# Kernel optimization log

Hardware: AMD Instinct MI355X
Metric: run time of the kernel (lower is better)

The kernel has to match this reference:

```python
import jax, jax.numpy as jnp
import numpy as np

VEC_SIZE = 256
N_VECS = 8
N_CHOICES = 2048
BATCH = 2048
EPS = 1e-6
NAND_BIAS = 3.0


def setup_inputs() -> dict:
    key = jax.random.key(0)
    k1, k2 = jax.random.split(key)
    query = jax.random.normal(k1, (BATCH, N_VECS * VEC_SIZE), dtype=jnp.float32)
    weight = jax.random.normal(k2, (N_CHOICES, VEC_SIZE * N_VECS), dtype=jnp.float32)
    # init code overwrites the randn nand_weight with ones + nand_bias
    nand_weight = jnp.full((N_CHOICES, N_VECS), 1.0 + NAND_BIAS, dtype=jnp.float32)
    return {"query": query, "weight": weight, "nand_weight": nand_weight}


def reference(query, weight, nand_weight):
    # [B, n_vecs, vec_size] and [C, n_vecs, vec_size]
    q = query.reshape(-1, N_VECS, VEC_SIZE)
    w = weight.reshape(-1, N_VECS, VEC_SIZE)
    # torch.cosine_similarity clamps each norm to eps
    qn = q / jnp.maximum(jnp.linalg.norm(q, axis=-1, keepdims=True), EPS)
    wn = w / jnp.maximum(jnp.linalg.norm(w, axis=-1, keepdims=True), EPS)
    # broadcast cosine sim expressed as batched matmul: [B, C, n_vecs]
    cos_sim = jnp.einsum('bnd,cnd->bcn', qn, wn)
    cos_sim = jax.nn.leaky_relu(cos_sim)  # slope 0.01, matches F.leaky_relu default
    nw = jax.nn.sigmoid(nand_weight)[None]  # [1, C, n_vecs]
    interpolated = nw * cos_sim + (1.0 - nw) * (1.0 - cos_sim)
    return jnp.prod(interpolated, axis=2)  # [B, C]
```

## Files before the change

### kernel.cpp

```cpp
#include <hip/hip_runtime.h>
#include <math.h>
#include <stdint.h>

#define BATCH    2048
#define NCHOICES 2048
#define NV       8
#define VS       256
#define KTOT     2048

typedef unsigned short u16;
typedef __attribute__((ext_vector_type(8))) short    bf16x8;
typedef __attribute__((ext_vector_type(8))) u16      u16x8;
typedef __attribute__((ext_vector_type(4))) float    f32x4;

__device__ __forceinline__ u16 f2bf_rne(float x) {
    unsigned u = __float_as_uint(x);
    return (u16)((u + 0x7FFFu + ((u >> 16) & 1u)) >> 16);
}

__global__ __launch_bounds__(256) void prep_convert(
    const float* __restrict__ Q, const float* __restrict__ W,
    const float* __restrict__ NWT,
    u16* __restrict__ Qh, u16* __restrict__ Ql,
    u16* __restrict__ Wh, u16* __restrict__ Wl,
    float* __restrict__ snw)
{
    const int row = blockIdx.x;
    const int t   = threadIdx.x;
    const int n   = t >> 5;
    const int l   = t & 31;

    const float* src; u16 *dh, *dl;
    if (row < BATCH) {
        src = Q + (size_t)row * KTOT;
        dh = Qh + (size_t)row * KTOT; dl = Ql + (size_t)row * KTOT;
    } else {
        src = W + (size_t)(row - BATCH) * KTOT;
        dh = Wh + (size_t)(row - BATCH) * KTOT; dl = Wl + (size_t)(row - BATCH) * KTOT;
    }

    const int idx = n * VS + l * 8;
    float4 x0 = *(const float4*)(src + idx);
    float4 x1 = *(const float4*)(src + idx + 4);
    float xs[8] = {x0.x, x0.y, x0.z, x0.w, x1.x, x1.y, x1.z, x1.w};

    float s = 0.0f;
    #pragma unroll
    for (int j = 0; j < 8; ++j) s = fmaf(xs[j], xs[j], s);
    #pragma unroll
    for (int m = 1; m < 32; m <<= 1) s += __shfl_xor(s, m, 64);
    const float rn = 1.0f / fmaxf(sqrtf(s), 1e-6f);

    u16x8 hv, lv;
    #pragma unroll
    for (int j = 0; j < 8; ++j) {
        float xn = xs[j] * rn;
        u16 h = f2bf_rne(xn);
        float hf = __uint_as_float(((unsigned)h) << 16);
        hv[j] = h;
        lv[j] = f2bf_rne(xn - hf);
    }
    *(u16x8*)(dh + idx) = hv;
    *(u16x8*)(dl + idx) = lv;

    if (row >= BATCH && t < NV) {
        const int c = row - BATCH;
        float x = NWT[(size_t)c * NV + t];
        snw[(size_t)c * NV + t] = 1.0f / (1.0f + expf(-x));
    }
}

__device__ __forceinline__ void gload16(const void* g, void* l) {
    __builtin_amdgcn_global_load_lds(
        (__attribute__((address_space(1))) void*)(uintptr_t)g,
        (__attribute__((address_space(3))) void*)(uint32_t)(uintptr_t)l,
        16, 0, 0);
}

#define RD16(dst, va, OFF) \
    asm volatile("ds_read_b128 %0, %1 offset:" OFF : "=v"(dst) : "v"(va))

__global__ __launch_bounds__(256, 2) void nand_mfma9(
    const u16* __restrict__ Qh, const u16* __restrict__ Ql,
    const u16* __restrict__ Wh, const u16* __restrict__ Wl,
    const float* __restrict__ snw, float* __restrict__ part)
{
    __shared__ __align__(16) u16 L[2][16384];

    const int tid  = threadIdx.x;
    const int lane = tid & 63;
    const int wave = tid >> 6;

    const int f    = blockIdx.x + 16 * blockIdx.y + 256 * blockIdx.z;
    const int virt = (f & 7) * 64 + (f >> 3);
    const int bx   = virt & 15;
    const int by   = (virt >> 4) & 15;
    const int z    = virt >> 8;

    const int wr  = (wave >> 1) * 64;
    const int wc  = (wave & 1) * 64;
    const int bm0 = by * 128;
    const int bn0 = bx * 128;
    const int kb  = z * 1024;

    const int fr = lane & 15;
    const int gi = lane >> 4;

    const int lr = lane >> 2;
    const int sw = 8 * ((lane & 3) ^ ((lane >> 3) & 3));
    const int r0 = wave * 32 + lr;
    const int r1 = r0 + 16;

    const u16* sAh0 = Qh + (size_t)(bm0 + r0) * KTOT + kb + sw;
    const u16* sAh1 = Qh + (size_t)(bm0 + r1) * KTOT + kb + sw;
    const u16* sAl0 = Ql + (size_t)(bm0 + r0) * KTOT + kb + sw;
    const u16* sAl1 = Ql + (size_t)(bm0 + r1) * KTOT + kb + sw;
    const u16* sBh0 = Wh + (size_t)(bn0 + r0) * KTOT + kb + sw;
    const u16* sBh1 = Wh + (size_t)(bn0 + r1) * KTOT + kb + sw;
    const u16* sBl0 = Wl + (size_t)(bn0 + r0) * KTOT + kb + sw;
    const u16* sBl1 = Wl + (size_t)(bn0 + r1) * KTOT + kb + sw;

    #define STAGE(B, T) do { u16* Lb_ = &L[B][0]; const int ko = (T) * 32;   \
        gload16(sAh0 + ko, Lb_ + wave * 1024);                               \
        gload16(sAh1 + ko, Lb_ + wave * 1024 + 512);                         \
        gload16(sAl0 + ko, Lb_ + 4096  + wave * 1024);                       \
        gload16(sAl1 + ko, Lb_ + 4096  + wave * 1024 + 512);                 \
        gload16(sBh0 + ko, Lb_ + 8192  + wave * 1024);                       \
        gload16(sBh1 + ko, Lb_ + 8192  + wave * 1024 + 512);                 \
        gload16(sBl0 + ko, Lb_ + 12288 + wave * 1024);                       \
        gload16(sBl1 + ko, Lb_ + 12288 + wave * 1024 + 512);                 \
    } while (0)

    const uint32_t ldsBase = (uint32_t)(uintptr_t)&L[0][0];
    const uint32_t swz16   = (uint32_t)((gi ^ ((fr >> 1) & 3)) * 16);
    const uint32_t vbaseA  = ldsBase + (uint32_t)((wr + fr) * 64) + swz16;
    const uint32_t vbaseB  = ldsBase + 16384u + (uint32_t)((wc + fr) * 64) + swz16;

    #define MF(AR, BR, M, N) \
        acc[M][N] = __builtin_amdgcn_mfma_f32_16x16x32_bf16(AR[M], BR[N], acc[M][N], 0, 0, 0)
    #define PASS(AR, BR) do {                                                \
        MF(AR, BR, 0, 0); MF(AR, BR, 0, 1); MF(AR, BR, 0, 2); MF(AR, BR, 0, 3); \
        MF(AR, BR, 1, 0); MF(AR, BR, 1, 1); MF(AR, BR, 1, 2); MF(AR, BR, 1, 3); \
        MF(AR, BR, 2, 0); MF(AR, BR, 2, 1); MF(AR, BR, 2, 2); MF(AR, BR, 2, 3); \
        MF(AR, BR, 3, 0); MF(AR, BR, 3, 1); MF(AR, BR, 3, 2); MF(AR, BR, 3, 3); \
    } while (0)

    f32x4 prod[4][4];
    #pragma unroll
    for (int m = 0; m < 4; ++m)
        #pragma unroll
        for (int n = 0; n < 4; ++n) prod[m][n] = (f32x4){1.f, 1.f, 1.f, 1.f};

    STAGE(0, 0);
    asm volatile("s_waitcnt vmcnt(0)");
    __builtin_amdgcn_s_barrier();

    int buf = 0;

    #pragma unroll 1
    for (int cc = 0; cc < 4; ++cc) {
        const int chunk = z * 4 + cc;

        f32x4 acc[4][4];
        #pragma unroll
        for (int m = 0; m < 4; ++m)
            #pragma unroll
            for (int n = 0; n < 4; ++n) acc[m][n] = (f32x4){0.f, 0.f, 0.f, 0.f};

        #pragma unroll 1
        for (int t8 = 0; t8 < 8; ++t8) {
            const int t = cc * 8 + t8;

            if (t + 1 < 32) STAGE(buf ^ 1, t + 1);

            const uint32_t vaA = vbaseA + ((uint32_t)buf << 15);
            const uint32_t vaB = vbaseB + ((uint32_t)buf << 15);

            bf16x8 ah[4], al[4], bh[4], bl[4];
            RD16(ah[0], vaA, "0");     RD16(bh[0], vaB, "0");
            RD16(ah[1], vaA, "1024");  RD16(bh[1], vaB, "1024");
            RD16(ah[2], vaA, "2048");  RD16(bh[2], vaB, "2048");
            RD16(ah[3], vaA, "3072");  RD16(bh[3], vaB, "3072");
            RD16(al[0], vaA, "8192");  RD16(al[1], vaA, "9216");
            RD16(al[2], vaA, "10240"); RD16(al[3], vaA, "11264");
            RD16(bl[0], vaB, "8192");  RD16(bl[1], vaB, "9216");
            RD16(bl[2], vaB, "10240"); RD16(bl[3], vaB, "11264");

            __builtin_amdgcn_s_setprio(1);
            asm volatile("s_waitcnt lgkmcnt(8)");
            __builtin_amdgcn_sched_barrier(0);
            PASS(ah, bh);
            __builtin_amdgcn_sched_barrier(0);
            asm volatile("s_waitcnt lgkmcnt(4)");
            __builtin_amdgcn_sched_barrier(0);
            PASS(al, bh);
            __builtin_amdgcn_sched_barrier(0);
            asm volatile("s_waitcnt lgkmcnt(0)");
            __builtin_amdgcn_sched_barrier(0);
            PASS(ah, bl);
            __builtin_amdgcn_s_setprio(0);

            asm volatile("s_waitcnt vmcnt(0)");
            __builtin_amdgcn_s_barrier();
            buf ^= 1;
        }

        float vv[4], uu[4];
        #pragma unroll
        for (int n = 0; n < 4; ++n) {
            const int col = bn0 + wc + n * 16 + fr;
            float s = snw[(size_t)col * NV + chunk];
            vv[n] = 2.0f * s - 1.0f;
            uu[n] = 1.0f - s;
        }
        #pragma unroll
        for (int m = 0; m < 4; ++m)
            #pragma unroll
            for (int i = 0; i < 4; ++i)
                #pragma unroll
                for (int n = 0; n < 4; ++n) {
                    float cosv = acc[m][n][i];
                    float Lk = fmaxf(cosv, 0.01f * cosv);
                    prod[m][n][i] *= fmaf(Lk, vv[n], uu[n]);
                }
    }

    const int ri = gi * 4;
    float* P = part + (size_t)z * BATCH * NCHOICES;
    #pragma unroll
    for (int m = 0; m < 4; ++m)
        #pragma unroll
        for (int i = 0; i < 4; ++i) {
            const int row = bm0 + wr + m * 16 + ri + i;
            float* pr = P + (size_t)row * NCHOICES + bn0 + wc + fr;
            #pragma unroll
            for (int n = 0; n < 4; ++n) pr[n * 16] = prod[m][n][i];
        }

    #undef STAGE
    #undef MF
    #undef PASS
}

__global__ __launch_bounds__(256) void combine_kernel(
    const float* __restrict__ p, float* __restrict__ out)
{
    const size_t NN = (size_t)BATCH * NCHOICES;
    size_t i = ((size_t)blockIdx.x * 256 + threadIdx.x) * 4;
    float4 a = *(const float4*)(p + i);
    float4 b = *(const float4*)(p + NN + i);
    float4 o;
    o.x = a.x * b.x;
    o.y = a.y * b.y;
    o.z = a.z * b.z;
    o.w = a.w * b.w;
    *(float4*)(out + i) = o;
}

__global__ __launch_bounds__(256) void prep_kernel(
    const float* __restrict__ Q, const float* __restrict__ W,
    const float* __restrict__ NWT,
    float* __restrict__ rq, float* __restrict__ rw, float* __restrict__ snw)
{
    const int row = blockIdx.x;
    const int t   = threadIdx.x;
    const int n   = t >> 5;
    const int l   = t & 31;

    const float* src; float* dst;
    if (row < BATCH) { src = Q + (size_t)row * KTOT; dst = rq + (size_t)row * NV; }
    else { src = W + (size_t)(row - BATCH) * KTOT; dst = rw + (size_t)(row - BATCH) * NV; }

    const float* v = src + n * VS + l * 8;
    float4 a = *(const float4*)(v);
    float4 b = *(const float4*)(v + 4);
    float s = a.x*a.x + a.y*a.y + a.z*a.z + a.w*a.w
            + b.x*b.x + b.y*b.y + b.z*b.z + b.w*b.w;
    #pragma unroll
    for (int m = 1; m < 32; m <<= 1) s += __shfl_xor(s, m, 64);
    if (l == 0) dst[n] = 1.0f / fmaxf(sqrtf(s), 1e-6f);
    if (row >= BATCH && t < NV) {
        const int c = row - BATCH;
        float x = NWT[(size_t)c * NV + t];
        snw[(size_t)c * NV + t] = 1.0f / (1.0f + expf(-x));
    }
}

__global__ __launch_bounds__(256, 2) void nand_gemm(
    const float* __restrict__ Q, const float* __restrict__ W,
    const float* __restrict__ rq, const float* __restrict__ rw,
    const float* __restrict__ snw, float* __restrict__ out)
{
    __shared__ __align__(16) float As[16][128 + 4];
    __shared__ __align__(16) float Bs[16][128 + 4];
    __shared__ __align__(16) float rqs[128];
    __shared__ __align__(16) float rws[128];
    __shared__ __align__(16) float sns[128];

    const int tid = threadIdx.x;
    const int tx  = tid & 15;
    const int ty  = tid >> 4;
    const int bm0 = blockIdx.y * 128;
    const int bn0 = blockIdx.x * 128;
    const int lr  = tid >> 2;
    const int lk  = (tid & 3) * 4;

    float prod[8][8];
    #pragma unroll
    for (int i = 0; i < 8; ++i)
        #pragma unroll
        for (int j = 0; j < 8; ++j) prod[i][j] = 1.0f;

    for (int n = 0; n < NV; ++n) {
        float acc[8][8];
        #pragma unroll
        for (int i = 0; i < 8; ++i)
            #pragma unroll
            for (int j = 0; j < 8; ++j) acc[i][j] = 0.0f;

        #pragma unroll 1
        for (int kt = 0; kt < VS / 16; ++kt) {
            const int k0 = n * VS + kt * 16;
            __syncthreads();
            {
                const float* qrow = Q + (size_t)(bm0 + lr) * KTOT + k0 + lk;
                float4 a0 = *(const float4*)(qrow);
                float4 a1 = *(const float4*)(qrow + (size_t)64 * KTOT);
                As[lk + 0][lr] = a0.x; As[lk + 1][lr] = a0.y;
                As[lk + 2][lr] = a0.z; As[lk + 3][lr] = a0.w;
                As[lk + 0][64 + lr] = a1.x; As[lk + 1][64 + lr] = a1.y;
                As[lk + 2][64 + lr] = a1.z; As[lk + 3][64 + lr] = a1.w;

                const float* wrow = W + (size_t)(bn0 + lr) * KTOT + k0 + lk;
                float4 b0 = *(const float4*)(wrow);
                float4 b1 = *(const float4*)(wrow + (size_t)64 * KTOT);
                Bs[lk + 0][lr] = b0.x; Bs[lk + 1][lr] = b0.y;
                Bs[lk + 2][lr] = b0.z; Bs[lk + 3][lr] = b0.w;
                Bs[lk + 0][64 + lr] = b1.x; Bs[lk + 1][64 + lr] = b1.y;
                Bs[lk + 2][64 + lr] = b1.z; Bs[lk + 3][64 + lr] = b1.w;
            }
            if (kt == 0) {
                for (int i = tid; i < 3 * 128; i += 256) {
                    if (i < 128)      rqs[i]       = rq[(size_t)(bm0 + i) * NV + n];
                    else if (i < 256) rws[i - 128] = rw[(size_t)(bn0 + i - 128) * NV + n];
                    else              sns[i - 256] = snw[(size_t)(bn0 + i - 256) * NV + n];
                }
            }
            __syncthreads();

            #pragma unroll
            for (int kk = 0; kk < 16; ++kk) {
                float4 a0 = *(const float4*)&As[kk][ty * 4];
                float4 a1 = *(const float4*)&As[kk][64 + ty * 4];
                float4 b0 = *(const float4*)&Bs[kk][tx * 4];
                float4 b1 = *(const float4*)&Bs[kk][64 + tx * 4];
                float ar[8] = {a0.x, a0.y, a0.z, a0.w, a1.x, a1.y, a1.z, a1.w};
                float br[8] = {b0.x, b0.y, b0.z, b0.w, b1.x, b1.y, b1.z, b1.w};
                #pragma unroll
                for (int i = 0; i < 8; ++i)
                    #pragma unroll
                    for (int j = 0; j < 8; ++j)
                        acc[i][j] = fmaf(ar[i], br[j], acc[i][j]);
            }
        }

        float rwv[8], uu[8], vv[8];
        #pragma unroll
        for (int j = 0; j < 8; ++j) {
            int cc = (j < 4) ? (tx * 4 + j) : (64 + tx * 4 + (j - 4));
            rwv[j] = rws[cc];
            float s = sns[cc];
            uu[j] = 1.0f - s;
            vv[j] = 2.0f * s - 1.0f;
        }
        #pragma unroll
        for (int i = 0; i < 8; ++i) {
            int r = (i < 4) ? (ty * 4 + i) : (64 + ty * 4 + (i - 4));
            float rqv = rqs[r];
            #pragma unroll
            for (int j = 0; j < 8; ++j) {
                float cosv = acc[i][j] * rqv * rwv[j];
                float Lk = fmaxf(cosv, 0.01f * cosv);
                prod[i][j] *= fmaf(Lk, vv[j], uu[j]);
            }
        }
    }

    #pragma unroll
    for (int i = 0; i < 8; ++i) {
        int r = (i < 4) ? (ty * 4 + i) : (64 + ty * 4 + (i - 4));
        float* orow = out + (size_t)(bm0 + r) * NCHOICES + bn0;
        float4 o0 = {prod[i][0], prod[i][1], prod[i][2], prod[i][3]};
        float4 o1 = {prod[i][4], prod[i][5], prod[i][6], prod[i][7]};
        *(float4*)(orow + tx * 4)      = o0;
        *(float4*)(orow + 64 + tx * 4) = o1;
    }
}

extern "C" void kernel_launch(void* const* d_in, const int* in_sizes, int n_in,
                              void* d_out, int out_size, void* d_ws, size_t ws_size,
                              hipStream_t stream)
{
    const float* Q   = (const float*)d_in[0];
    const float* W   = (const float*)d_in[1];
    const float* NWT = (const float*)d_in[2];
    float* out = (float*)d_out;

    char* w = (char*)d_ws;
    float* rq  = (float*)w; w += (size_t)BATCH    * NV * 4;
    float* rwn = (float*)w; w += (size_t)NCHOICES * NV * 4;
    float* snw = (float*)w; w += (size_t)NCHOICES * NV * 4;
    u16* Qh = (u16*)w; w += (size_t)BATCH * KTOT * 2;
    u16* Ql = (u16*)w; w += (size_t)BATCH * KTOT * 2;
    u16* Wh = (u16*)w; w += (size_t)NCHOICES * KTOT * 2;
    u16* Wl = (u16*)w; w += (size_t)NCHOICES * KTOT * 2;
    float* part = (float*)w; w += (size_t)2 * BATCH * NCHOICES * 4;
    const size_t needed = (size_t)(w - (char*)d_ws);

    if (ws_size >= needed) {
        prep_convert<<<BATCH + NCHOICES, 256, 0, stream>>>(
            Q, W, NWT, Qh, Ql, Wh, Wl, snw);
        dim3 grid(NCHOICES / 128, BATCH / 128, 2);
        nand_mfma9<<<grid, 256, 0, stream>>>(Qh, Ql, Wh, Wl, snw, part);
        combine_kernel<<<(BATCH * NCHOICES / 4) / 256, 256, 0, stream>>>(part, out);
    } else {
        prep_kernel<<<BATCH + NCHOICES, 256, 0, stream>>>(Q, W, NWT, rq, rwn, snw);
        dim3 grid(NCHOICES / 128, BATCH / 128);
        nand_gemm<<<grid, 256, 0, stream>>>(Q, W, rq, rwn, snw, out);
    }
}
```

Before: 77.74 us.

## Widen GEMM tile to 128x256 with 8 waves and triple-buffered LDS pipeline

Replaces the 4-wave 128x128 tile kernel with an 8-wave 128x256 tile. Each A tile is now reused across twice as many output columns. The LDS double buffer becomes a three-stage ring that prefetches two k-steps ahead with partial vmcnt waits, and the nested chunk loop is flattened into one loop that runs the per-chunk epilogue inline. The sigmoid weights are now prefetched one step before each chunk's epilogue. In exchange the block uses 144KB of LDS, which limits residency, and the grid is halved to 256 blocks, which may underfill the CUs.

```diff
diff --git a/kernel.cpp b/kernel.cpp
--- a/kernel.cpp
+++ b/kernel.cpp
@@ -80,55 +80,71 @@
 #define RD16(dst, va, OFF) \
     asm volatile("ds_read_b128 %0, %1 offset:" OFF : "=v"(dst) : "v"(va))
 
-__global__ __launch_bounds__(256, 2) void nand_mfma9(
+#define GLD_F32(dst, p) \
+    asm volatile("global_load_dword %0, %1, off" : "=v"(dst) : "v"(p))
+
+__device__ __forceinline__ void chunk_epi(f32x4 (&acc)[4][4], f32x4 (&prod)[4][4],
+                                          float sn0, float sn1, float sn2, float sn3)
+{
+    float vvv[4] = {2.f*sn0-1.f, 2.f*sn1-1.f, 2.f*sn2-1.f, 2.f*sn3-1.f};
+    float uuu[4] = {1.f-sn0, 1.f-sn1, 1.f-sn2, 1.f-sn3};
+    #pragma unroll
+    for (int m = 0; m < 4; ++m)
+        #pragma unroll
+        for (int i = 0; i < 4; ++i)
+            #pragma unroll
+            for (int n = 0; n < 4; ++n) {
+                float cosv = acc[m][n][i];
+                float Lk = fmaxf(cosv, 0.01f * cosv);
+                prod[m][n][i] *= fmaf(Lk, vvv[n], uuu[n]);
+                acc[m][n][i] = 0.f;
+            }
+}
+
+__global__ __launch_bounds__(512, 2) void nand_mfma10(
     const u16* __restrict__ Qh, const u16* __restrict__ Ql,
     const u16* __restrict__ Wh, const u16* __restrict__ Wl,
     const float* __restrict__ snw, float* __restrict__ part)
 {
-    __shared__ __align__(16) u16 L[2][16384];
+    __shared__ __align__(16) u16 L[3][24576];
 
     const int tid  = threadIdx.x;
     const int lane = tid & 63;
     const int wave = tid >> 6;
 
-    const int f    = blockIdx.x + 16 * blockIdx.y + 256 * blockIdx.z;
-    const int virt = (f & 7) * 64 + (f >> 3);
-    const int bx   = virt & 15;
-    const int by   = (virt >> 4) & 15;
-    const int z    = virt >> 8;
-
-    const int wr  = (wave >> 1) * 64;
-    const int wc  = (wave & 1) * 64;
+    const int f    = blockIdx.x + 8 * blockIdx.y + 128 * blockIdx.z;
+    const int virt = (f & 7) * 32 + (f >> 3);
+    const int bx   = virt & 7;
+    const int by   = (virt >> 3) & 15;
+    const int z    = virt >> 7;
+
+    const int wr  = (wave >> 2) * 64;
+    const int wc  = (wave & 3) * 64;
     const int bm0 = by * 128;
-    const int bn0 = bx * 128;
+    const int bn0 = bx * 256;
     const int kb  = z * 1024;
 
     const int fr = lane & 15;
     const int gi = lane >> 4;
 
-    const int lr = lane >> 2;
-    const int sw = 8 * ((lane & 3) ^ ((lane >> 3) & 3));
-    const int r0 = wave * 32 + lr;
-    const int r1 = r0 + 16;
-
-    const u16* sAh0 = Qh + (size_t)(bm0 + r0) * KTOT + kb + sw;
-    const u16* sAh1 = Qh + (size_t)(bm0 + r1) * KTOT + kb + sw;
-    const u16* sAl0 = Ql + (size_t)(bm0 + r0) * KTOT + kb + sw;
-    const u16* sAl1 = Ql + (size_t)(bm0 + r1) * KTOT + kb + sw;
-    const u16* sBh0 = Wh + (size_t)(bn0 + r0) * KTOT + kb + sw;
-    const u16* sBh1 = Wh + (size_t)(bn0 + r1) * KTOT + kb + sw;
-    const u16* sBl0 = Wl + (size_t)(bn0 + r0) * KTOT + kb + sw;
-    const u16* sBl1 = Wl + (size_t)(bn0 + r1) * KTOT + kb + sw;
-
-    #define STAGE(B, T) do { u16* Lb_ = &L[B][0]; const int ko = (T) * 32;   \
-        gload16(sAh0 + ko, Lb_ + wave * 1024);                               \
-        gload16(sAh1 + ko, Lb_ + wave * 1024 + 512);                         \
-        gload16(sAl0 + ko, Lb_ + 4096  + wave * 1024);                       \
-        gload16(sAl1 + ko, Lb_ + 4096  + wave * 1024 + 512);                 \
-        gload16(sBh0 + ko, Lb_ + 8192  + wave * 1024);                       \
-        gload16(sBh1 + ko, Lb_ + 8192  + wave * 1024 + 512);                 \
-        gload16(sBl0 + ko, Lb_ + 12288 + wave * 1024);                       \
-        gload16(sBl1 + ko, Lb_ + 12288 + wave * 1024 + 512);                 \
+    const int gr = tid >> 2;
+    const int sw = 8 * ((tid & 3) ^ ((gr >> 1) & 3));
+
+    const u16* sAh  = Qh + (size_t)(bm0 + gr) * KTOT + kb + sw;
+    const u16* sAl  = Ql + (size_t)(bm0 + gr) * KTOT + kb + sw;
+    const u16* sBh0 = Wh + (size_t)(bn0 + gr) * KTOT + kb + sw;
+    const u16* sBh1 = Wh + (size_t)(bn0 + 128 + gr) * KTOT + kb + sw;
+    const u16* sBl0 = Wl + (size_t)(bn0 + gr) * KTOT + kb + sw;
+    const u16* sBl1 = Wl + (size_t)(bn0 + 128 + gr) * KTOT + kb + sw;
+
+    #define STAGE(SOFFU, T) do {                                             \
+        u16* Lb_ = ((u16*)L) + (SOFFU); const int ko = (T) * 32;             \
+        gload16(sAh  + ko, Lb_ + tid * 8);                                   \
+        gload16(sAl  + ko, Lb_ + 4096  + tid * 8);                           \
+        gload16(sBh0 + ko, Lb_ + 8192  + tid * 8);                           \
+        gload16(sBh1 + ko, Lb_ + 12288 + tid * 8);                           \
+        gload16(sBl0 + ko, Lb_ + 16384 + tid * 8);                           \
+        gload16(sBl1 + ko, Lb_ + 20480 + tid * 8);                           \
     } while (0)
 
     const uint32_t ldsBase = (uint32_t)(uintptr_t)&L[0][0];
@@ -145,84 +161,92 @@
         MF(AR, BR, 3, 0); MF(AR, BR, 3, 1); MF(AR, BR, 3, 2); MF(AR, BR, 3, 3); \
     } while (0)
 
-    f32x4 prod[4][4];
+    #define TILE_COMPUTE(VAA, VAB) do {                                      \
+        RD16(ah[0], VAA, "0");     RD16(bh[0], VAB, "0");                    \
+        RD16(ah[1], VAA, "1024");  RD16(bh[1], VAB, "1024");                 \
+        RD16(ah[2], VAA, "2048");  RD16(bh[2], VAB, "2048");                 \
+        RD16(ah[3], VAA, "3072");  RD16(bh[3], VAB, "3072");                 \
+        RD16(al[0], VAA, "8192");  RD16(al[1], VAA, "9216");                 \
+        RD16(al[2], VAA, "10240"); RD16(al[3], VAA, "11264");                \
+        RD16(bl[0], VAB, "16384"); RD16(bl[1], VAB, "17408");                \
+        RD16(bl[2], VAB, "18432"); RD16(bl[3], VAB, "19456");                \
+        __builtin_amdgcn_s_setprio(1);                                       \
+        asm volatile("s_waitcnt lgkmcnt(8)");                                \
+        __builtin_amdgcn_sched_barrier(0);                                   \
+        PASS(ah, bh);                                                        \
+        __builtin_amdgcn_sched_barrier(0);                                   \
+        asm volatile("s_waitcnt lgkmcnt(4)");                                \
+        __builtin_amdgcn_sched_barrier(0);                                   \
+        PASS(al, bh);                                                        \
+        __builtin_amdgcn_sched_barrier(0);                                   \
+        asm volatile("s_waitcnt lgkmcnt(0)");                                \
+        __builtin_amdgcn_sched_barrier(0);                                   \
+        PASS(ah, bl);                                                        \
+        __builtin_amdgcn_s_setprio(0);                                       \
+    } while (0)
+
+    bf16x8 ah[4], al[4], bh[4], bl[4];
+    f32x4 acc[4][4], prod[4][4];
+    float sn0, sn1, sn2, sn3;
     #pragma unroll
     for (int m = 0; m < 4; ++m)
         #pragma unroll
-        for (int n = 0; n < 4; ++n) prod[m][n] = (f32x4){1.f, 1.f, 1.f, 1.f};
+        for (int n = 0; n < 4; ++n) {
+            acc[m][n]  = (f32x4){0.f, 0.f, 0.f, 0.f};
+            prod[m][n] = (f32x4){1.f, 1.f, 1.f, 1.f};
+        }
+
+    const float* snwBase = snw + (size_t)(bn0 + wc + fr) * NV + z * 4;
 
     STAGE(0, 0);
-    asm volatile("s_waitcnt vmcnt(0)");
+    STAGE(24576, 1);
+    asm volatile("s_waitcnt vmcnt(6)");
     __builtin_amdgcn_s_barrier();
 
-    int buf = 0;
+    uint32_t rOffB = 0;
+    uint32_t sOffU = 49152;
 
     #pragma unroll 1
-    for (int cc = 0; cc < 4; ++cc) {
-        const int chunk = z * 4 + cc;
-
-        f32x4 acc[4][4];
-        #pragma unroll
-        for (int m = 0; m < 4; ++m)
-            #pragma unroll
-            for (int n = 0; n < 4; ++n) acc[m][n] = (f32x4){0.f, 0.f, 0.f, 0.f};
-
-        #pragma unroll 1
-        for (int t8 = 0; t8 < 8; ++t8) {
-            const int t = cc * 8 + t8;
-
-            if (t + 1 < 32) STAGE(buf ^ 1, t + 1);
-
-            const uint32_t vaA = vbaseA + ((uint32_t)buf << 15);
-            const uint32_t vaB = vbaseB + ((uint32_t)buf << 15);
-
-            bf16x8 ah[4], al[4], bh[4], bl[4];
-            RD16(ah[0], vaA, "0");     RD16(bh[0], vaB, "0");
-            RD16(ah[1], vaA, "1024");  RD16(bh[1], vaB, "1024");
-            RD16(ah[2], vaA, "2048");  RD16(bh[2], vaB, "2048");
-            RD16(ah[3], vaA, "3072");  RD16(bh[3], vaB, "3072");
-            RD16(al[0], vaA, "8192");  RD16(al[1], vaA, "9216");
-            RD16(al[2], vaA, "10240"); RD16(al[3], vaA, "11264");
-            RD16(bl[0], vaB, "8192");  RD16(bl[1], vaB, "9216");
-            RD16(bl[2], vaB, "10240"); RD16(bl[3], vaB, "11264");
-
-            __builtin_amdgcn_s_setprio(1);
-            asm volatile("s_waitcnt lgkmcnt(8)");
+    for (int t = 0; t < 30; ++t) {
+        if ((t & 7) == 7) {
+            const float* snwP = snwBase + (t >> 3);
+            GLD_F32(sn0, snwP);       GLD_F32(sn1, snwP + 128);
+            GLD_F32(sn2, snwP + 256); GLD_F32(sn3, snwP + 384);
             __builtin_amdgcn_sched_barrier(0);
-            PASS(ah, bh);
-            __builtin_amdgcn_sched_barrier(0);
-            asm volatile("s_waitcnt lgkmcnt(4)");
-            __builtin_amdgcn_sched_barrier(0);
-            PASS(al, bh);
-            __builtin_amdgcn_sched_barrier(0);
-            asm volatile("s_waitcnt lgkmcnt(0)");
-            __builtin_amdgcn_sched_barrier(0);
-            PASS(ah, bl);
-            __builtin_amdgcn_s_setprio(0);
-
-            asm volatile("s_waitcnt vmcnt(0)");
-            __builtin_amdgcn_s_barrier();
-            buf ^= 1;
-        }
-
-        float vv[4], uu[4];
-        #pragma unroll
-        for (int n = 0; n < 4; ++n) {
-            const int col = bn0 + wc + n * 16 + fr;
-            float s = snw[(size_t)col * NV + chunk];
-            vv[n] = 2.0f * s - 1.0f;
-            uu[n] = 1.0f - s;
-        }
-        #pragma unroll
-        for (int m = 0; m < 4; ++m)
-            #pragma unroll
-            for (int i = 0; i < 4; ++i)
-                #pragma unroll
-                for (int n = 0; n < 4; ++n) {
-                    float cosv = acc[m][n][i];
-                    float Lk = fmaxf(cosv, 0.01f * cosv);
-                    prod[m][n][i] *= fmaf(Lk, vv[n], uu[n]);
-                }
+        }
+        STAGE(sOffU, t + 2);
+
+        const uint32_t vaA = vbaseA + rOffB;
+        const uint32_t vaB = vbaseB + rOffB;
+        TILE_COMPUTE(vaA, vaB);
+
+        asm volatile("s_waitcnt vmcnt(6)");
+        __builtin_amdgcn_s_barrier();
+
+        rOffB += 49152u; if (rOffB == 147456u) rOffB = 0;
+        sOffU += 24576u; if (sOffU == 73728u)  sOffU = 0;
+
+        if ((t & 7) == 7) chunk_epi(acc, prod, sn0, sn1, sn2, sn3);
+    }
+    {
+        const uint32_t vaA = vbaseA + rOffB;
+        const uint32_t vaB = vbaseB + rOffB;
+        TILE_COMPUTE(vaA, vaB);
+        asm volatile("s_waitcnt vmcnt(0)");
+        __builtin_amdgcn_s_barrier();
+        rOffB += 49152u; if (rOffB == 147456u) rOffB = 0;
+    }
+    {
+        const float* snwP = snwBase + 3;
+        GLD_F32(sn0, snwP);       GLD_F32(sn1, snwP + 128);
+        GLD_F32(sn2, snwP + 256); GLD_F32(sn3, snwP + 384);
+        __builtin_amdgcn_sched_barrier(0);
+        const uint32_t vaA = vbaseA + rOffB;
+        const uint32_t vaB = vbaseB + rOffB;
+        TILE_COMPUTE(vaA, vaB);
+        asm volatile("s_waitcnt vmcnt(0)");
+        __builtin_amdgcn_sched_barrier(0);
+        chunk_epi(acc, prod, sn0, sn1, sn2, sn3);
     }
 
     const int ri = gi * 4;
@@ -240,6 +264,7 @@
     #undef STAGE
     #undef MF
     #undef PASS
+    #undef TILE_COMPUTE
 }
 
 __global__ __launch_bounds__(256) void combine_kernel(
@@ -420,8 +445,8 @@
     if (ws_size >= needed) {
         prep_convert<<<BATCH + NCHOICES, 256, 0, stream>>>(
             Q, W, NWT, Qh, Ql, Wh, Wl, snw);
-        dim3 grid(NCHOICES / 128, BATCH / 128, 2);
-        nand_mfma9<<<grid, 256, 0, stream>>>(Qh, Ql, Wh, Wl, snw, part);
+        dim3 grid(NCHOICES / 256, BATCH / 128, 2);
+        nand_mfma10<<<grid, 512, 0, stream>>>(Qh, Ql, Wh, Wl, snw, part);
         combine_kernel<<<(BATCH * NCHOICES / 4) / 256, 256, 0, stream>>>(part, out);
     } else {
         prep_kernel<<<BATCH + NCHOICES, 256, 0, stream>>>(Q, W, NWT, rq, rwn, snw);
```

New measurement: 75.74 us. 2.6% less time.
